# Kernel optimization log

Hardware: AMD Instinct MI355X
Metric: run time of the kernel (lower is better)

Reference implementation:

```python
import jax, jax.numpy as jnp
import numpy as np

E = 4          # num_experts
C = 64         # emb_size
HID = 2 * C    # hidden_rate * emb_size
TOP_K = 2
BN_EPS = 1e-5
B, HH, WW = 16, 128, 128


def setup_inputs() -> dict:
    key = jax.random.key(0)
    ks = jax.random.split(key, 8)
    s = 0.05
    inp = {
        'x':  jax.random.normal(ks[0], (B, C, HH, WW), jnp.float32),
        # expert conv weights stacked over expert dim (1x1 convs -> plain matrices)
        'W1': jax.random.normal(ks[1], (E, HID, C), jnp.float32) * s,
        'b1': jnp.zeros((E, HID), jnp.float32),
        'g1': jnp.ones((E, HID), jnp.float32),
        'be1': jnp.zeros((E, HID), jnp.float32),
        'm1': jnp.zeros((E, HID), jnp.float32),
        'v1': jnp.ones((E, HID), jnp.float32),
        'W2': jax.random.normal(ks[2], (E, HID, HID), jnp.float32) * s,
        'b2': jnp.zeros((E, HID), jnp.float32),
        'g2': jnp.ones((E, HID), jnp.float32),
        'be2': jnp.zeros((E, HID), jnp.float32),
        'm2': jnp.zeros((E, HID), jnp.float32),
        'v2': jnp.ones((E, HID), jnp.float32),
        'W3': jax.random.normal(ks[3], (E, C, HID), jnp.float32) * s,
        'b3': jnp.zeros((E, C), jnp.float32),
        'gw': jax.random.normal(ks[4], (E, C), jnp.float32) * s,  # gate Linear weight
        'gb': jnp.zeros((E,), jnp.float32),                        # gate Linear bias
    }
    return inp


def _bn(h, g, b, m, v):
    # h: (B,E,K,H,W); per-expert, per-channel BatchNorm in eval mode (running stats)
    inv = g / jnp.sqrt(v + BN_EPS)
    return h * inv[None, :, :, None, None] + (b - m * inv)[None, :, :, None, None]


def _cv_squared(u):
    eps = 1e-10
    mean = jnp.mean(u)
    var = jnp.mean((u - mean) ** 2)  # unbiased=False
    return var / (mean ** 2 + eps)


def reference(x, W1, b1, g1, be1, m1, v1, W2, b2, g2, be2, m2, v2, W3, b3, gw, gb):
    b = x.shape[0]
    # gate on global-average-pooled features
    gap = jnp.mean(x, axis=(2, 3))                      # (B,C)
    logits = gap @ gw.T + gb                            # (B,E)
    probs = jax.nn.softmax(logits, axis=-1)
    _, top_idx = jax.lax.top_k(probs, TOP_K)            # (B,k)
    mask = jnp.zeros_like(probs).at[jnp.arange(b)[:, None], top_idx].set(1.0)
    gated = probs * mask
    gated = gated / (jnp.sum(gated, axis=-1, keepdims=True) + 1e-8)  # (B,E)

    # all experts densely (faithful to original), 1x1 convs as channel GEMMs
    h = jnp.einsum('eoc,bcxy->beoxy', W1, x) + b1[None, :, :, None, None]
    h = jax.nn.relu(_bn(h, g1, be1, m1, v1))
    h = jnp.einsum('eoi,beixy->beoxy', W2, h) + b2[None, :, :, None, None]
    h = jax.nn.relu(_bn(h, g2, be2, m2, v2))
    eo = jnp.einsum('eci,beixy->becxy', W3, h) + b3[None, :, :, None, None]  # (B,E,C,H,W)

    out = jnp.einsum('be,becxy->bcxy', gated, eo)       # weighted combine
    aux_loss = _cv_squared(jnp.sum(gated, axis=0))      # (E,) usage -> scalar
    return out, aux_loss
```

## Files before the change

kernel.cpp:

```cpp
#include <hip/hip_runtime.h>
#include <hip/hip_bf16.h>

#define HWsz 16384
#define Cdim 64
#define HIDd 128
#define NEXP 4
#define NBAT 16

typedef _Float16 h8 __attribute__((ext_vector_type(8)));
typedef _Float16 h4 __attribute__((ext_vector_type(4)));
typedef float f4 __attribute__((ext_vector_type(4)));

#define OFF_W1F 0
#define OFF_W2F 65536
#define OFF_W3F 196608
#define OFF_B1F 262144
#define OFF_B2F 264192
#define OFF_B3F 266240
#define OFF_GAP 267264
#define OFF_GIDX 271360
#define OFF_GW  271488

__device__ __forceinline__ void pinv(f4& v) { asm volatile("" : "+v"(v)); }

__global__ void prep_k(const float* __restrict__ x, float* __restrict__ gap,
                       const float* __restrict__ W1, const float* __restrict__ b1,
                       const float* __restrict__ g1, const float* __restrict__ be1,
                       const float* __restrict__ m1, const float* __restrict__ v1,
                       const float* __restrict__ W2, const float* __restrict__ b2,
                       const float* __restrict__ g2, const float* __restrict__ be2,
                       const float* __restrict__ m2, const float* __restrict__ v2,
                       const float* __restrict__ W3, const float* __restrict__ b3,
                       _Float16* __restrict__ W1f, _Float16* __restrict__ W2f,
                       _Float16* __restrict__ W3f,
                       float* __restrict__ b1f, float* __restrict__ b2f,
                       float* __restrict__ b3f)
{
  const int t = threadIdx.x;
  if (blockIdx.x < 1024) {
    const int bc = blockIdx.x;
    const float* p = x + (size_t)bc * HWsz;
    float s = 0.f;
    for (int i = t; i < HWsz / 4; i += 256) {
      const float4 v = ((const float4*)p)[i];
      s += v.x + v.y + v.z + v.w;
    }
    for (int off = 32; off; off >>= 1) s += __shfl_down(s, off, 64);
    __shared__ float red[4];
    if ((t & 63) == 0) red[t >> 6] = s;
    __syncthreads();
    if (t == 0) gap[bc] = (red[0] + red[1] + red[2] + red[3]) * (1.0f / HWsz);
  } else {
    const int i = (blockIdx.x - 1024) * 256 + t;
    if (i < 32768) {
      const int eo = i >> 6;
      const float inv = g1[eo] * rsqrtf(v1[eo] + 1e-5f);
      W1f[i] = (_Float16)(W1[i] * inv);
    } else if (i < 98304) {
      const int j = i - 32768;
      const int eo = j >> 7;
      const float inv = g2[eo] * rsqrtf(v2[eo] + 1e-5f);
      W2f[j] = (_Float16)(W2[j] * inv);
    } else if (i < 131072) {
      const int k = i - 98304;
      W3f[k] = (_Float16)W3[k];
    } else if (i < 131584) {
      const int l = i - 131072;
      const float inv = g1[l] * rsqrtf(v1[l] + 1e-5f);
      b1f[l] = b1[l] * inv + be1[l] - m1[l] * inv;
    } else if (i < 132096) {
      const int l = i - 131584;
      const float inv = g2[l] * rsqrtf(v2[l] + 1e-5f);
      b2f[l] = b2[l] * inv + be2[l] - m2[l] * inv;
    } else if (i < 132352) {
      b3f[i - 132096] = b3[i - 132096];
    }
  }
}

__global__ void gate_k(const float* __restrict__ gap, const float* __restrict__ gwt,
                       const float* __restrict__ gb, int* __restrict__ gidx,
                       float* __restrict__ gwo, float* __restrict__ aux)
{
  const int t = threadIdx.x;
  __shared__ float logits[NBAT][NEXP];
  __shared__ float gated[NBAT][NEXP];
  {
    const int b = t >> 2, e = t & 3;
    float s = gb[e];
    for (int c = 0; c < Cdim; c++) s += gap[b * Cdim + c] * gwt[e * Cdim + c];
    logits[b][e] = s;
  }
  __syncthreads();
  if (t < NBAT) {
    const int b = t;
    float p[NEXP];
    float mx = logits[b][0];
    for (int e = 1; e < NEXP; e++) mx = fmaxf(mx, logits[b][e]);
    float sum = 0.f;
    for (int e = 0; e < NEXP; e++) { p[e] = expf(logits[b][e] - mx); sum += p[e]; }
    for (int e = 0; e < NEXP; e++) p[e] /= sum;
    int i0 = 0;
    for (int e = 1; e < NEXP; e++) if (p[e] > p[i0]) i0 = e;
    int i1 = (i0 == 0) ? 1 : 0;
    for (int e = 0; e < NEXP; e++) if (e != i0 && p[e] > p[i1]) i1 = e;
    const float s2 = p[i0] + p[i1] + 1e-8f;
    const float w0 = p[i0] / s2, w1 = p[i1] / s2;
    gidx[2 * b] = i0; gidx[2 * b + 1] = i1;
    gwo[2 * b] = w0;  gwo[2 * b + 1] = w1;
    for (int e = 0; e < NEXP; e++)
      gated[b][e] = (e == i0) ? w0 : ((e == i1) ? w1 : 0.f);
  }
  __syncthreads();
  if (t == 0) {
    float imp[NEXP] = {0.f, 0.f, 0.f, 0.f};
    for (int b = 0; b < NBAT; b++)
      for (int e = 0; e < NEXP; e++) imp[e] += gated[b][e];
    float mean = 0.f;
    for (int e = 0; e < NEXP; e++) mean += imp[e];
    mean *= 0.25f;
    float var = 0.f;
    for (int e = 0; e < NEXP; e++) { const float d = imp[e] - mean; var += d * d; }
    var *= 0.25f;
    aux[0] = var / (mean * mean + 1e-10f);
  }
}

__global__ __launch_bounds__(256, 2)
void moe_main_k(const float* __restrict__ x, float* __restrict__ out,
                const _Float16* __restrict__ W1f, const _Float16* __restrict__ W2f,
                const _Float16* __restrict__ W3f,
                const float* __restrict__ b1f, const float* __restrict__ b2f,
                const float* __restrict__ b3f,
                const int* __restrict__ gidx, const float* __restrict__ gwv)
{
  __shared__ __align__(16) _Float16 Xs[2][64][72];
  __shared__ __align__(16) _Float16 H1[2][64][136];
  __shared__ __align__(16) _Float16 H2[64][136];
  __shared__ __align__(16) float    bias_lds[2][320];

  const int bx = blockIdx.x;
  const int b  = bx >> 7;
  const int n0 = (bx & 127) << 7;
  const int t  = threadIdx.x;
  const int w  = t >> 6;
  const int lane = t & 63;
  const int ln = lane & 15;
  const int q  = lane >> 4;
  const int mh = w >> 1;
  const int nh = w & 1;

  const int   ea0 = gidx[2 * b], ea1 = gidx[2 * b + 1];
  const float wa0 = gwv[2 * b],  wa1 = gwv[2 * b + 1];

  for (int i = t; i < 640; i += 256) {
    const int sl = i >= 320;
    const int j  = i - (sl ? 320 : 0);
    const int e  = sl ? ea1 : ea0;
    float v;
    if (j < 128)      v = b1f[e * HIDd + j];
    else if (j < 256) v = b2f[e * HIDd + (j - 128)];
    else              v = b3f[e * Cdim + (j - 256)];
    bias_lds[sl][j] = v;
  }

  {
    const int c0 = t >> 4;
    const int n4 = (t & 15) << 2;
    const float* xb = x + (size_t)b * (Cdim * HWsz) + n0;
#pragma unroll
    for (int tt = 0; tt < 2; tt++)
#pragma unroll
      for (int ci = 0; ci < 4; ci++) {
        const int c = c0 + (ci << 4);
        const float4 v = *(const float4*)(xb + (size_t)c * HWsz + (tt << 6) + n4);
        Xs[tt][n4 + 0][c] = (_Float16)v.x;
        Xs[tt][n4 + 1][c] = (_Float16)v.y;
        Xs[tt][n4 + 2][c] = (_Float16)v.z;
        Xs[tt][n4 + 3][c] = (_Float16)v.w;
      }
  }

  f4 oacc[2][2][2];
#pragma unroll
  for (int tt = 0; tt < 2; tt++)
#pragma unroll
    for (int i = 0; i < 2; i++)
#pragma unroll
      for (int j = 0; j < 2; j++)
        oacc[tt][i][j] = f4{0.f, 0.f, 0.f, 0.f};

  __syncthreads();

#pragma unroll 1
  for (int slot = 0; slot < 2; slot++) {
    const int   e  = slot ? ea1 : ea0;
    const float we = slot ? wa1 : wa0;
    const _Float16* w1 = W1f + e * (HIDd * Cdim);
    const _Float16* w2 = W2f + e * (HIDd * HIDd);
    const _Float16* w3 = W3f + e * (Cdim * HIDd);

    f4 A1[4][2], A2[4][4], A3[2][4];
#pragma unroll
    for (int mi = 0; mi < 4; mi++) {
      const int m0 = (((mh << 2) + mi) << 4);
      const _Float16* p1 = w1 + (m0 + ln) * Cdim + q * 8;
      A1[mi][0] = *(const f4*)(p1);
      A1[mi][1] = *(const f4*)(p1 + 32);
      const _Float16* p2 = w2 + (m0 + ln) * HIDd + q * 8;
#pragma unroll
      for (int ks = 0; ks < 4; ks++) A2[mi][ks] = *(const f4*)(p2 + ks * 32);
    }
#pragma unroll
    for (int mi = 0; mi < 2; mi++) {
      const int m0 = (((mh << 1) + mi) << 4);
      const _Float16* p3 = w3 + (m0 + ln) * HIDd + q * 8;
#pragma unroll
      for (int ks = 0; ks < 4; ks++) A3[mi][ks] = *(const f4*)(p3 + ks * 32);
    }
#pragma unroll
    for (int mi = 0; mi < 4; mi++) {
      pinv(A1[mi][0]); pinv(A1[mi][1]);
#pragma unroll
      for (int ks = 0; ks < 4; ks++) pinv(A2[mi][ks]);
    }
#pragma unroll
    for (int mi = 0; mi < 2; mi++)
#pragma unroll
      for (int ks = 0; ks < 4; ks++) pinv(A3[mi][ks]);

    auto L1 = [&](int tb) {
#pragma unroll
      for (int ni = 0; ni < 2; ni++) {
        const int nrow = ((nh << 1) + ni) * 16 + ln;
        const h8 bf0 = *(const h8*)&Xs[tb][nrow][q * 8];
        const h8 bf1 = *(const h8*)&Xs[tb][nrow][32 + q * 8];
        __builtin_amdgcn_s_setprio(1);
#pragma unroll
        for (int mi = 0; mi < 4; mi++) {
          const int m0 = (((mh << 2) + mi) << 4);
          f4 acc = {0.f, 0.f, 0.f, 0.f};
          acc = __builtin_amdgcn_mfma_f32_16x16x32_f16(__builtin_bit_cast(h8, A1[mi][0]), bf0, acc, 0, 0, 0);
          acc = __builtin_amdgcn_mfma_f32_16x16x32_f16(__builtin_bit_cast(h8, A1[mi][1]), bf1, acc, 0, 0, 0);
          const f4 bias = *(const f4*)&bias_lds[slot][m0 + q * 4];
          h4 hv;
#pragma unroll
          for (int r = 0; r < 4; r++) hv[r] = (_Float16)fmaxf(acc[r] + bias[r], 0.f);
          *(h4*)&H1[tb][nrow][m0 + q * 4] = hv;
        }
        __builtin_amdgcn_s_setprio(0);
      }
    };
    auto L2 = [&](int tb) {
#pragma unroll
      for (int ni = 0; ni < 2; ni++) {
        const int nrow = ((nh << 1) + ni) * 16 + ln;
        h8 bf[4];
#pragma unroll
        for (int ks = 0; ks < 4; ks++) bf[ks] = *(const h8*)&H1[tb][nrow][ks * 32 + q * 8];
        __builtin_amdgcn_s_setprio(1);
#pragma unroll
        for (int mi = 0; mi < 4; mi++) {
          const int m0 = (((mh << 2) + mi) << 4);
          f4 acc = {0.f, 0.f, 0.f, 0.f};
#pragma unroll
          for (int ks = 0; ks < 4; ks++)
            acc = __builtin_amdgcn_mfma_f32_16x16x32_f16(__builtin_bit_cast(h8, A2[mi][ks]), bf[ks], acc, 0, 0, 0);
          const f4 bias = *(const f4*)&bias_lds[slot][128 + m0 + q * 4];
          h4 hv;
#pragma unroll
          for (int r = 0; r < 4; r++) hv[r] = (_Float16)fmaxf(acc[r] + bias[r], 0.f);
          *(h4*)&H2[nrow][m0 + q * 4] = hv;
        }
        __builtin_amdgcn_s_setprio(0);
      }
    };
    auto L3 = [&](int tb) {
#pragma unroll
      for (int ni = 0; ni < 2; ni++) {
        const int nrow = ((nh << 1) + ni) * 16 + ln;
        h8 bf[4];
#pragma unroll
        for (int ks = 0; ks < 4; ks++) bf[ks] = *(const h8*)&H2[nrow][ks * 32 + q * 8];
        __builtin_amdgcn_s_setprio(1);
#pragma unroll
        for (int mi = 0; mi < 2; mi++) {
          const int m0 = (((mh << 1) + mi) << 4);
          f4 acc = {0.f, 0.f, 0.f, 0.f};
#pragma unroll
          for (int ks = 0; ks < 4; ks++)
            acc = __builtin_amdgcn_mfma_f32_16x16x32_f16(__builtin_bit_cast(h8, A3[mi][ks]), bf[ks], acc, 0, 0, 0);
          const f4 bias = *(const f4*)&bias_lds[slot][256 + m0 + q * 4];
#pragma unroll
          for (int r = 0; r < 4; r++) oacc[tb][mi][ni][r] += we * (acc[r] + bias[r]);
        }
        __builtin_amdgcn_s_setprio(0);
      }
    };

    L1(0);
    __syncthreads();
    L2(0); L1(1);
    __syncthreads();
    L3(0);
    __syncthreads();
    L2(1);
    __syncthreads();
    L3(1);
  }

#pragma unroll
  for (int tl = 0; tl < 2; tl++)
#pragma unroll
    for (int mi = 0; mi < 2; mi++)
#pragma unroll
      for (int ni = 0; ni < 2; ni++) {
        const int c = ((mh << 1) + mi) * 16 + q * 4;
        const int n = n0 + (tl << 6) + ((nh << 1) + ni) * 16 + ln;
#pragma unroll
        for (int r = 0; r < 4; r++)
          __builtin_nontemporal_store(oacc[tl][mi][ni][r],
                                      &out[((size_t)(b * Cdim + c + r)) * HWsz + n]);
      }
}

extern "C" void kernel_launch(void* const* d_in, const int* in_sizes, int n_in,
                              void* d_out, int out_size, void* d_ws, size_t ws_size,
                              hipStream_t stream)
{
  const float* x   = (const float*)d_in[0];
  const float* W1  = (const float*)d_in[1];
  const float* b1  = (const float*)d_in[2];
  const float* g1  = (const float*)d_in[3];
  const float* be1 = (const float*)d_in[4];
  const float* m1  = (const float*)d_in[5];
  const float* v1  = (const float*)d_in[6];
  const float* W2  = (const float*)d_in[7];
  const float* b2  = (const float*)d_in[8];
  const float* g2  = (const float*)d_in[9];
  const float* be2 = (const float*)d_in[10];
  const float* m2  = (const float*)d_in[11];
  const float* v2  = (const float*)d_in[12];
  const float* W3  = (const float*)d_in[13];
  const float* b3  = (const float*)d_in[14];
  const float* gwt = (const float*)d_in[15];
  const float* gb  = (const float*)d_in[16];

  char* ws = (char*)d_ws;
  _Float16* W1f = (_Float16*)(ws + OFF_W1F);
  _Float16* W2f = (_Float16*)(ws + OFF_W2F);
  _Float16* W3f = (_Float16*)(ws + OFF_W3F);
  float* b1f = (float*)(ws + OFF_B1F);
  float* b2f = (float*)(ws + OFF_B2F);
  float* b3f = (float*)(ws + OFF_B3F);
  float* gap = (float*)(ws + OFF_GAP);
  int*   gidx = (int*)(ws + OFF_GIDX);
  float* gwo = (float*)(ws + OFF_GW);

  float* out = (float*)d_out;
  float* aux = out + (size_t)NBAT * Cdim * HWsz;

  hipLaunchKernelGGL(prep_k, dim3(1542), dim3(256), 0, stream,
                     x, gap, W1, b1, g1, be1, m1, v1, W2, b2, g2, be2, m2, v2,
                     W3, b3, W1f, W2f, W3f, b1f, b2f, b3f);
  hipLaunchKernelGGL(gate_k, dim3(1), dim3(64), 0, stream, gap, gwt, gb, gidx, gwo, aux);
  hipLaunchKernelGGL(moe_main_k, dim3(2048), dim3(256), 0, stream,
                     x, out, W1f, W2f, W3f, b1f, b2f, b3f, gidx, gwo);
}
```

Before: 223.8 us.

## Fold gate into prep via last-block atomic, swizzle LDS, raise occupancy

The separate gate kernel is removed. The last block to finish the global-average-pool reduction, detected with an atomic counter that is reset by a memset, now computes the gating. The GAP loop is unrolled into four independent accumulators. In the main kernel the padded LDS arrays become XOR-swizzled unpadded buffers, H1 is no longer double buffered, and the stage order is reworked so LDS shrinks and launch bounds can rise to 3 blocks per CU. Pinning of the A1/A3 weight registers is dropped and x is loaded as scalar per-channel reads. Risks are register spills at the higher occupancy and the extra memset launch.

New measurement: 467.8 us. 2.09x slower.

```diff
diff --git a/kernel.cpp b/kernel.cpp
--- a/kernel.cpp
+++ b/kernel.cpp
@@ -20,6 +20,7 @@
 #define OFF_GAP 267264
 #define OFF_GIDX 271360
 #define OFF_GW  271488
+#define OFF_CNT 271616
 
 __device__ __forceinline__ void pinv(f4& v) { asm volatile("" : "+v"(v)); }
 
@@ -34,22 +35,84 @@
                        _Float16* __restrict__ W1f, _Float16* __restrict__ W2f,
                        _Float16* __restrict__ W3f,
                        float* __restrict__ b1f, float* __restrict__ b2f,
-                       float* __restrict__ b3f)
+                       float* __restrict__ b3f,
+                       const float* __restrict__ gwt, const float* __restrict__ gb,
+                       int* __restrict__ gidx, float* __restrict__ gwo,
+                       float* __restrict__ aux, int* __restrict__ cnt)
 {
   const int t = threadIdx.x;
   if (blockIdx.x < 1024) {
     const int bc = blockIdx.x;
-    const float* p = x + (size_t)bc * HWsz;
-    float s = 0.f;
-    for (int i = t; i < HWsz / 4; i += 256) {
-      const float4 v = ((const float4*)p)[i];
-      s += v.x + v.y + v.z + v.w;
-    }
+    const float4* p4 = (const float4*)(x + (size_t)bc * HWsz);
+    float s0 = 0.f, s1 = 0.f, s2 = 0.f, s3 = 0.f;
+#pragma unroll
+    for (int i = t; i < 4096; i += 1024) {
+      const float4 a = p4[i], b4 = p4[i + 256], c4 = p4[i + 512], d4 = p4[i + 768];
+      s0 += a.x + a.y + a.z + a.w;
+      s1 += b4.x + b4.y + b4.z + b4.w;
+      s2 += c4.x + c4.y + c4.z + c4.w;
+      s3 += d4.x + d4.y + d4.z + d4.w;
+    }
+    float s = s0 + s1 + s2 + s3;
     for (int off = 32; off; off >>= 1) s += __shfl_down(s, off, 64);
     __shared__ float red[4];
+    __shared__ int lastFlag;
     if ((t & 63) == 0) red[t >> 6] = s;
     __syncthreads();
-    if (t == 0) gap[bc] = (red[0] + red[1] + red[2] + red[3]) * (1.0f / HWsz);
+    if (t == 0) {
+      const float val = (red[0] + red[1] + red[2] + red[3]) * (1.0f / HWsz);
+      __hip_atomic_store(&gap[bc], val, __ATOMIC_RELEASE, __HIP_MEMORY_SCOPE_AGENT);
+      const int old = __hip_atomic_fetch_add(cnt, 1, __ATOMIC_ACQ_REL, __HIP_MEMORY_SCOPE_AGENT);
+      lastFlag = (old == 1023) ? 1 : 0;
+    }
+    __syncthreads();
+    if (lastFlag) {
+      __shared__ float logits[NBAT][NEXP];
+      __shared__ float gated[NBAT][NEXP];
+      if (t < 64) {
+        const int b = t >> 2, e = t & 3;
+        float s2g = gb[e];
+        for (int c = 0; c < Cdim; c++) {
+          const float gv = __hip_atomic_load(&gap[b * Cdim + c], __ATOMIC_RELAXED,
+                                             __HIP_MEMORY_SCOPE_AGENT);
+          s2g += gv * gwt[e * Cdim + c];
+        }
+        logits[b][e] = s2g;
+      }
+      __syncthreads();
+      if (t < NBAT) {
+        const int b = t;
+        float p[NEXP];
+        float mx = logits[b][0];
+        for (int e = 1; e < NEXP; e++) mx = fmaxf(mx, logits[b][e]);
+        float sum = 0.f;
+        for (int e = 0; e < NEXP; e++) { p[e] = expf(logits[b][e] - mx); sum += p[e]; }
+        for (int e = 0; e < NEXP; e++) p[e] /= sum;
+        int i0 = 0;
+        for (int e = 1; e < NEXP; e++) if (p[e] > p[i0]) i0 = e;
+        int i1 = (i0 == 0) ? 1 : 0;
+        for (int e = 0; e < NEXP; e++) if (e != i0 && p[e] > p[i1]) i1 = e;
+        const float s2 = p[i0] + p[i1] + 1e-8f;
+        const float w0 = p[i0] / s2, w1 = p[i1] / s2;
+        gidx[2 * b] = i0; gidx[2 * b + 1] = i1;
+        gwo[2 * b] = w0;  gwo[2 * b + 1] = w1;
+        for (int e = 0; e < NEXP; e++)
+          gated[b][e] = (e == i0) ? w0 : ((e == i1) ? w1 : 0.f);
+      }
+      __syncthreads();
+      if (t == 0) {
+        float imp[NEXP] = {0.f, 0.f, 0.f, 0.f};
+        for (int b = 0; b < NBAT; b++)
+          for (int e = 0; e < NEXP; e++) imp[e] += gated[b][e];
+        float mean = 0.f;
+        for (int e = 0; e < NEXP; e++) mean += imp[e];
+        mean *= 0.25f;
+        float var = 0.f;
+        for (int e = 0; e < NEXP; e++) { const float d = imp[e] - mean; var += d * d; }
+        var *= 0.25f;
+        aux[0] = var / (mean * mean + 1e-10f);
+      }
+    }
   } else {
     const int i = (blockIdx.x - 1024) * 256 + t;
     if (i < 32768) {
@@ -78,55 +141,7 @@
   }
 }
 
-__global__ void gate_k(const float* __restrict__ gap, const float* __restrict__ gwt,
-                       const float* __restrict__ gb, int* __restrict__ gidx,
-                       float* __restrict__ gwo, float* __restrict__ aux)
-{
-  const int t = threadIdx.x;
-  __shared__ float logits[NBAT][NEXP];
-  __shared__ float gated[NBAT][NEXP];
-  {
-    const int b = t >> 2, e = t & 3;
-    float s = gb[e];
-    for (int c = 0; c < Cdim; c++) s += gap[b * Cdim + c] * gwt[e * Cdim + c];
-    logits[b][e] = s;
-  }
-  __syncthreads();
-  if (t < NBAT) {
-    const int b = t;
-    float p[NEXP];
-    float mx = logits[b][0];
-    for (int e = 1; e < NEXP; e++) mx = fmaxf(mx, logits[b][e]);
-    float sum = 0.f;
-    for (int e = 0; e < NEXP; e++) { p[e] = expf(logits[b][e] - mx); sum += p[e]; }
-    for (int e = 0; e < NEXP; e++) p[e] /= sum;
-    int i0 = 0;
-    for (int e = 1; e < NEXP; e++) if (p[e] > p[i0]) i0 = e;
-    int i1 = (i0 == 0) ? 1 : 0;
-    for (int e = 0; e < NEXP; e++) if (e != i0 && p[e] > p[i1]) i1 = e;
-    const float s2 = p[i0] + p[i1] + 1e-8f;
-    const float w0 = p[i0] / s2, w1 = p[i1] / s2;
-    gidx[2 * b] = i0; gidx[2 * b + 1] = i1;
-    gwo[2 * b] = w0;  gwo[2 * b + 1] = w1;
-    for (int e = 0; e < NEXP; e++)
-      gated[b][e] = (e == i0) ? w0 : ((e == i1) ? w1 : 0.f);
-  }
-  __syncthreads();
-  if (t == 0) {
-    float imp[NEXP] = {0.f, 0.f, 0.f, 0.f};
-    for (int b = 0; b < NBAT; b++)
-      for (int e = 0; e < NEXP; e++) imp[e] += gated[b][e];
-    float mean = 0.f;
-    for (int e = 0; e < NEXP; e++) mean += imp[e];
-    mean *= 0.25f;
-    float var = 0.f;
-    for (int e = 0; e < NEXP; e++) { const float d = imp[e] - mean; var += d * d; }
-    var *= 0.25f;
-    aux[0] = var / (mean * mean + 1e-10f);
-  }
-}
-
-__global__ __launch_bounds__(256, 2)
+__global__ __launch_bounds__(256, 3)
 void moe_main_k(const float* __restrict__ x, float* __restrict__ out,
                 const _Float16* __restrict__ W1f, const _Float16* __restrict__ W2f,
                 const _Float16* __restrict__ W3f,
@@ -134,9 +149,9 @@
                 const float* __restrict__ b3f,
                 const int* __restrict__ gidx, const float* __restrict__ gwv)
 {
-  __shared__ __align__(16) _Float16 Xs[2][64][72];
-  __shared__ __align__(16) _Float16 H1[2][64][136];
-  __shared__ __align__(16) _Float16 H2[64][136];
+  __shared__ __align__(16) _Float16 Xs[2][64 * 64];
+  __shared__ __align__(16) _Float16 H1s[64 * 128];
+  __shared__ __align__(16) _Float16 H2s[64 * 128];
   __shared__ __align__(16) float    bias_lds[2][320];
 
   const int bx = blockIdx.x;
@@ -165,20 +180,25 @@
   }
 
   {
-    const int c0 = t >> 4;
-    const int n4 = (t & 15) << 2;
-    const float* xb = x + (size_t)b * (Cdim * HWsz) + n0;
-#pragma unroll
-    for (int tt = 0; tt < 2; tt++)
-#pragma unroll
-      for (int ci = 0; ci < 4; ci++) {
-        const int c = c0 + (ci << 4);
-        const float4 v = *(const float4*)(xb + (size_t)c * HWsz + (tt << 6) + n4);
-        Xs[tt][n4 + 0][c] = (_Float16)v.x;
-        Xs[tt][n4 + 1][c] = (_Float16)v.y;
-        Xs[tt][n4 + 2][c] = (_Float16)v.z;
-        Xs[tt][n4 + 3][c] = (_Float16)v.w;
-      }
+    const int pos = t & 63;
+    const int cb  = (t >> 6) << 4;
+    const int sw  = (pos & 7) << 4;
+    const float* xb = x + (size_t)b * (Cdim * HWsz) + n0 + pos;
+#pragma unroll
+    for (int tt = 0; tt < 2; tt++) {
+      const float* xc = xb + (tt << 6);
+#pragma unroll
+      for (int j = 0; j < 4; j++) {
+        const int c = cb + (j << 2);
+        const float v0 = xc[(size_t)(c + 0) * HWsz];
+        const float v1 = xc[(size_t)(c + 1) * HWsz];
+        const float v2 = xc[(size_t)(c + 2) * HWsz];
+        const float v3 = xc[(size_t)(c + 3) * HWsz];
+        h4 hv; hv[0] = (_Float16)v0; hv[1] = (_Float16)v1;
+               hv[2] = (_Float16)v2; hv[3] = (_Float16)v3;
+        *(h4*)((char*)&Xs[tt][0] + pos * 128 + (((c << 1)) ^ sw)) = hv;
+      }
+    }
   }
 
   f4 oacc[2][2][2];
@@ -219,22 +239,17 @@
       for (int ks = 0; ks < 4; ks++) A3[mi][ks] = *(const f4*)(p3 + ks * 32);
     }
 #pragma unroll
-    for (int mi = 0; mi < 4; mi++) {
-      pinv(A1[mi][0]); pinv(A1[mi][1]);
+    for (int mi = 0; mi < 4; mi++)
 #pragma unroll
       for (int ks = 0; ks < 4; ks++) pinv(A2[mi][ks]);
-    }
-#pragma unroll
-    for (int mi = 0; mi < 2; mi++)
-#pragma unroll
-      for (int ks = 0; ks < 4; ks++) pinv(A3[mi][ks]);
 
     auto L1 = [&](int tb) {
 #pragma unroll
       for (int ni = 0; ni < 2; ni++) {
         const int nrow = ((nh << 1) + ni) * 16 + ln;
-        const h8 bf0 = *(const h8*)&Xs[tb][nrow][q * 8];
-        const h8 bf1 = *(const h8*)&Xs[tb][nrow][32 + q * 8];
+        const int sw = (nrow & 7) << 4;
+        const h8 bf0 = *(const h8*)((const char*)&Xs[tb][0] + nrow * 128 + ((q * 16) ^ sw));
+        const h8 bf1 = *(const h8*)((const char*)&Xs[tb][0] + nrow * 128 + ((64 + q * 16) ^ sw));
         __builtin_amdgcn_s_setprio(1);
 #pragma unroll
         for (int mi = 0; mi < 4; mi++) {
@@ -246,18 +261,20 @@
           h4 hv;
 #pragma unroll
           for (int r = 0; r < 4; r++) hv[r] = (_Float16)fmaxf(acc[r] + bias[r], 0.f);
-          *(h4*)&H1[tb][nrow][m0 + q * 4] = hv;
+          *(h4*)((char*)H1s + nrow * 256 + (((m0 << 1) + (q << 3)) ^ sw)) = hv;
         }
         __builtin_amdgcn_s_setprio(0);
       }
     };
-    auto L2 = [&](int tb) {
+    auto L2 = [&]() {
 #pragma unroll
       for (int ni = 0; ni < 2; ni++) {
         const int nrow = ((nh << 1) + ni) * 16 + ln;
+        const int sw = (nrow & 7) << 4;
         h8 bf[4];
 #pragma unroll
-        for (int ks = 0; ks < 4; ks++) bf[ks] = *(const h8*)&H1[tb][nrow][ks * 32 + q * 8];
+        for (int ks = 0; ks < 4; ks++)
+          bf[ks] = *(const h8*)((const char*)H1s + nrow * 256 + (((ks << 6) + (q << 4)) ^ sw));
         __builtin_amdgcn_s_setprio(1);
 #pragma unroll
         for (int mi = 0; mi < 4; mi++) {
@@ -270,7 +287,7 @@
           h4 hv;
 #pragma unroll
           for (int r = 0; r < 4; r++) hv[r] = (_Float16)fmaxf(acc[r] + bias[r], 0.f);
-          *(h4*)&H2[nrow][m0 + q * 4] = hv;
+          *(h4*)((char*)H2s + nrow * 256 + (((m0 << 1) + (q << 3)) ^ sw)) = hv;
         }
         __builtin_amdgcn_s_setprio(0);
       }
@@ -279,9 +296,11 @@
 #pragma unroll
       for (int ni = 0; ni < 2; ni++) {
         const int nrow = ((nh << 1) + ni) * 16 + ln;
+        const int sw = (nrow & 7) << 4;
         h8 bf[4];
 #pragma unroll
-        for (int ks = 0; ks < 4; ks++) bf[ks] = *(const h8*)&H2[nrow][ks * 32 + q * 8];
+        for (int ks = 0; ks < 4; ks++)
+          bf[ks] = *(const h8*)((const char*)H2s + nrow * 256 + (((ks << 6) + (q << 4)) ^ sw));
         __builtin_amdgcn_s_setprio(1);
 #pragma unroll
         for (int mi = 0; mi < 2; mi++) {
@@ -300,13 +319,14 @@
 
     L1(0);
     __syncthreads();
-    L2(0); L1(1);
-    __syncthreads();
-    L3(0);
-    __syncthreads();
-    L2(1);
+    L2();
+    __syncthreads();
+    L3(0); L1(1);
+    __syncthreads();
+    L2();
     __syncthreads();
     L3(1);
+    __syncthreads();
   }
 
 #pragma unroll
@@ -356,14 +376,16 @@
   float* gap = (float*)(ws + OFF_GAP);
   int*   gidx = (int*)(ws + OFF_GIDX);
   float* gwo = (float*)(ws + OFF_GW);
+  int*   cnt = (int*)(ws + OFF_CNT);
 
   float* out = (float*)d_out;
   float* aux = out + (size_t)NBAT * Cdim * HWsz;
 
+  hipMemsetAsync(cnt, 0, 4, stream);
   hipLaunchKernelGGL(prep_k, dim3(1542), dim3(256), 0, stream,
                      x, gap, W1, b1, g1, be1, m1, v1, W2, b2, g2, be2, m2, v2,
-                     W3, b3, W1f, W2f, W3f, b1f, b2f, b3f);
-  hipLaunchKernelGGL(gate_k, dim3(1), dim3(64), 0, stream, gap, gwt, gb, gidx, gwo, aux);
+                     W3, b3, W1f, W2f, W3f, b1f, b2f, b3f,
+                     gwt, gb, gidx, gwo, aux, cnt);
   hipLaunchKernelGGL(moe_main_k, dim3(2048), dim3(256), 0, stream,
                      x, out, W1f, W2f, W3f, b1f, b2f, b3f, gidx, gwo);
 }
```
